# Kernel tuning notes

Hardware: AMD Instinct MI355X
Metric: run time of the kernel (lower is better)

Reference implementation:

```python
import jax, jax.numpy as jnp
import numpy as np

N = 50000
E = 800000
IN_DIM = 6
HID = 32
HEADS = 2
NEG_SLOPE = 0.2


def setup_inputs() -> dict:
    key = jax.random.key(0)
    ks = jax.random.split(key, 12)
    x = jax.random.normal(ks[0], (N, IN_DIM), dtype=jnp.float32)
    edge_index = jax.random.randint(ks[1], (2, E), 0, N, dtype=jnp.int64)
    s = 0.1
    W1 = jax.random.normal(ks[2], (IN_DIM, HEADS * HID), jnp.float32) * s
    a_src1 = jax.random.normal(ks[3], (HEADS, HID), jnp.float32) * s
    a_dst1 = jax.random.normal(ks[4], (HEADS, HID), jnp.float32) * s
    b1 = jnp.zeros((HEADS * HID,), jnp.float32)
    W2 = jax.random.normal(ks[5], (HEADS * HID, HID), jnp.float32) * s
    a_src2 = jax.random.normal(ks[6], (1, HID), jnp.float32) * s
    a_dst2 = jax.random.normal(ks[7], (1, HID), jnp.float32) * s
    b2 = jnp.zeros((HID,), jnp.float32)
    Wout = jax.random.normal(ks[8], (HID, 1), jnp.float32) * s
    bout = jnp.zeros((1,), jnp.float32)
    return {"x": x, "edge_index": edge_index, "W1": W1, "a_src1": a_src1,
            "a_dst1": a_dst1, "b1": b1, "W2": W2, "a_src2": a_src2,
            "a_dst2": a_dst2, "b2": b2, "Wout": Wout, "bout": bout}


def gat_conv(x, src, dst, n, W, a_src, a_dst, b, heads, out_ch, concat):
    # x: [N, F_in]; src/dst: [E'] (self-loops already appended)
    h = (x @ W).reshape(n, heads, out_ch)              # [N, H, C]
    alpha_s = jnp.sum(h * a_src, axis=-1)              # [N, H]
    alpha_d = jnp.sum(h * a_dst, axis=-1)              # [N, H]
    e = jax.nn.leaky_relu(alpha_s[src] + alpha_d[dst], NEG_SLOPE)  # [E', H]
    # segment softmax over incoming edges of each destination node
    m = jax.ops.segment_max(e, dst, num_segments=n)    # [N, H]
    ex = jnp.exp(e - m[dst])
    denom = jax.ops.segment_sum(ex, dst, num_segments=n)
    alpha = ex / denom[dst]                            # [E', H]
    out = jax.ops.segment_sum(alpha[:, :, None] * h[src], dst, num_segments=n)  # [N, H, C]
    out = out.reshape(n, heads * out_ch) if concat else out.mean(axis=1)
    return out + b


def reference(x, edge_index, W1, a_src1, a_dst1, b1, W2, a_src2, a_dst2, b2, Wout, bout):
    n = x.shape[0]
    loops = jnp.arange(n, dtype=edge_index.dtype)
    src = jnp.concatenate([edge_index[0], loops])
    dst = jnp.concatenate([edge_index[1], loops])
    h = jax.nn.relu(gat_conv(x, src, dst, n, W1, a_src1, a_dst1, b1, HEADS, HID, True))
    h = jax.nn.relu(gat_conv(h, src, dst, n, W2, a_src2, a_dst2, b2, 1, HID, False))
    return jax.nn.sigmoid(h @ Wout + bout).squeeze(-1)  # [N]
```

## Files before the change

kernel.cpp:

```cpp
#include <hip/hip_runtime.h>
#include <hip/hip_fp16.h>

#define N_NODES 50000
#define N_EDGES 800000
#define ETOT    (N_EDGES + N_NODES)
#define NEG_SLOPE 0.2f
#define NBIN    ((N_NODES + 255) / 256)
#define CHUNK   4096
#define B_COARSE ((ETOT + CHUNK - 1) / CHUNK)
#define G_NODE1 ((N_NODES + 3) / 4)
#define NG1     (N_NODES / 16)

__device__ __forceinline__ float leaky(float v) {
    return v > 0.f ? v : NEG_SLOPE * v;
}

__device__ __forceinline__ void edge_src_dst(const int* ei, int e, int& src, int& dst) {
    if (e < N_EDGES) { src = ei[e]; dst = ei[N_EDGES + e]; }
    else             { src = dst = e - N_EDGES; }
}

__global__ void k_pre(const float* __restrict__ x, const float* __restrict__ W1,
                      const float* __restrict__ a_src1, const float* __restrict__ a_dst1,
                      float* __restrict__ xs1, float* __restrict__ ad1,
                      const int* __restrict__ ei, int* __restrict__ bh) {
    __shared__ int h[NBIN];
    if (blockIdx.x < G_NODE1) {
        int node = blockIdx.x * 4 + (threadIdx.x >> 6);
        if (node >= N_NODES) return;
        int j = threadIdx.x & 63;
        int head = j >> 5;
        float xk[6];
#pragma unroll
        for (int k = 0; k < 6; ++k)
            xk[k] = x[node * 6 + k];
        float hv = 0.f;
#pragma unroll
        for (int k = 0; k < 6; ++k)
            hv += xk[k] * W1[k * 64 + j];
        float s = hv * a_src1[j];
        float d = hv * a_dst1[j];
#pragma unroll
        for (int m = 1; m < 32; m <<= 1) {
            s += __shfl_xor(s, m);
            d += __shfl_xor(d, m);
        }
        if ((j & 31) == 0) {
            xs1[node * 8 + head] = s;
            ad1[node * 2 + head] = d;
        }
        if (j >= 2 && j < 8)
            xs1[node * 8 + j] = xk[j - 2];
    } else {
        int b = blockIdx.x - G_NODE1;
        for (int i = threadIdx.x; i < NBIN; i += 256) h[i] = 0;
        __syncthreads();
        int base = b * CHUNK;
        int lim = min(base + CHUNK, ETOT);
        for (int e = base + threadIdx.x; e < lim; e += 256) {
            int s, d; edge_src_dst(ei, e, s, d);
            atomicAdd(&h[d >> 8], 1);
        }
        __syncthreads();
        for (int i = threadIdx.x; i < NBIN; i += 256)
            bh[b * NBIN + i] = h[i];
    }
}

__global__ void k_cscan_a(int* __restrict__ bh, int* __restrict__ bintot) {
    __shared__ int s[256];
    int bin = blockIdx.x;
    int t = threadIdx.x;
    int v = (t < B_COARSE) ? bh[t * NBIN + bin] : 0;
    int x = v;
    s[t] = x;
    __syncthreads();
#pragma unroll
    for (int o = 1; o < 256; o <<= 1) {
        int tt = (t >= o) ? s[t - o] : 0;
        __syncthreads();
        x += tt;
        s[t] = x;
        __syncthreads();
    }
    if (t < B_COARSE) bh[t * NBIN + bin] = x - v;
    if (t == 255) bintot[bin] = x;
}

__global__ void k_cscan_b(const int* __restrict__ bintot, int* __restrict__ binoff) {
    __shared__ int s[256];
    int t = threadIdx.x;
    int v = (t < NBIN) ? bintot[t] : 0;
    int x = v;
    s[t] = x;
    __syncthreads();
#pragma unroll
    for (int o = 1; o < 256; o <<= 1) {
        int tt = (t >= o) ? s[t - o] : 0;
        __syncthreads();
        x += tt;
        s[t] = x;
        __syncthreads();
    }
    if (t < NBIN) binoff[t] = x - v;
    if (t == 255) binoff[NBIN] = x;
}

__global__ void k_cscatter(const int* __restrict__ ei, const int* __restrict__ bh,
                           const int* __restrict__ binoff, unsigned* __restrict__ ebin) {
    __shared__ int cur[NBIN];
    for (int i = threadIdx.x; i < NBIN; i += 256)
        cur[i] = bh[blockIdx.x * NBIN + i] + binoff[i];
    __syncthreads();
    int base = blockIdx.x * CHUNK;
    int lim = min(base + CHUNK, ETOT);
    for (int e = base + threadIdx.x; e < lim; e += 256) {
        int s, d; edge_src_dst(ei, e, s, d);
        int pos = atomicAdd(&cur[d >> 8], 1);
        ebin[pos] = ((unsigned)s << 8) | (unsigned)(d & 255);
    }
}

__global__ void k_fine(const unsigned* __restrict__ ebin, const int* __restrict__ binoff,
                       int* __restrict__ rowstart, int* __restrict__ csr_src) {
    __shared__ int h[256];
    __shared__ int cur[256];
    int bin = blockIdx.x;
    int beg = binoff[bin], end = binoff[bin + 1];
    int t = threadIdx.x;
    h[t] = 0;
    __syncthreads();
    for (int i = beg + t; i < end; i += 256)
        atomicAdd(&h[ebin[i] & 255u], 1);
    __syncthreads();
    int v = h[t];
    int x = v;
    cur[t] = x;
    __syncthreads();
#pragma unroll
    for (int o = 1; o < 256; o <<= 1) {
        int tt = (t >= o) ? cur[t - o] : 0;
        __syncthreads();
        x += tt;
        cur[t] = x;
        __syncthreads();
    }
    int start = beg + x - v;
    int node = bin * 256 + t;
    if (node < N_NODES) rowstart[node] = start;
    if (bin == NBIN - 1 && t == 0) rowstart[N_NODES] = ETOT;
    cur[t] = start;
    __syncthreads();
    for (int i = beg + t; i < end; i += 256) {
        unsigned p = ebin[i];
        int pos = atomicAdd(&cur[p & 255u], 1);
        csr_src[pos] = (int)(p >> 8);
    }
}

__global__ void k_gat12(const int* __restrict__ csr_src, const int* __restrict__ rowstart,
                        const float* __restrict__ xs1, const float* __restrict__ ad1,
                        const float* __restrict__ W1, const float* __restrict__ b1,
                        const float* __restrict__ W2, const float* __restrict__ as_w2,
                        const float* __restrict__ ad_w2, __half* __restrict__ h2h,
                        float* __restrict__ as2, float* __restrict__ ad2) {
    __shared__ float W2s[64 * 32];
    __shared__ float o1s[16 * 66];
    int t = threadIdx.x;
    for (int i = t; i < 64 * 32; i += 256)
        W2s[i] = W2[i];

    int l = t & 15;
    int ln = t >> 4;
    int node = blockIdx.x * 16 + ln;

    float p[4][6];
    float bv[4];
#pragma unroll
    for (int m = 0; m < 4; ++m) {
        int c = l + 16 * m;
#pragma unroll
        for (int k = 0; k < 6; ++k)
            p[m][k] = W1[k * 64 + c];
        bv[m] = b1[c];
    }

    int beg = rowstart[node], end = rowstart[node + 1];
    float2 adv = ((const float2*)ad1)[node];

    float a0 = 0, a1 = 0, a2 = 0, a3 = 0, a4 = 0, a5 = 0;
    float c0 = 0, c1 = 0, c2 = 0, c3 = 0, c4 = 0, c5 = 0;
    float dp0 = 0, dp1 = 0;
    for (int i = beg + l; i < end; i += 16) {
        int s = csr_src[i];
        const float4* xp = (const float4*)(xs1 + (size_t)s * 8);
        float4 A = xp[0], B = xp[1];
        float w0 = __expf(leaky(A.x + adv.x));
        float w1 = __expf(leaky(A.y + adv.y));
        dp0 += w0;
        dp1 += w1;
        a0 += w0 * A.z; a1 += w0 * A.w; a2 += w0 * B.x;
        a3 += w0 * B.y; a4 += w0 * B.z; a5 += w0 * B.w;
        c0 += w1 * A.z; c1 += w1 * A.w; c2 += w1 * B.x;
        c3 += w1 * B.y; c4 += w1 * B.z; c5 += w1 * B.w;
    }
#pragma unroll
    for (int o = 8; o; o >>= 1) {
        a0 += __shfl_xor(a0, o); a1 += __shfl_xor(a1, o); a2 += __shfl_xor(a2, o);
        a3 += __shfl_xor(a3, o); a4 += __shfl_xor(a4, o); a5 += __shfl_xor(a5, o);
        c0 += __shfl_xor(c0, o); c1 += __shfl_xor(c1, o); c2 += __shfl_xor(c2, o);
        c3 += __shfl_xor(c3, o); c4 += __shfl_xor(c4, o); c5 += __shfl_xor(c5, o);
        dp0 += __shfl_xor(dp0, o); dp1 += __shfl_xor(dp1, o);
    }
    float inv0 = 1.f / dp0;
    float inv1 = 1.f / dp1;
#pragma unroll
    for (int m = 0; m < 4; ++m) {
        float dot;
        if (m < 2)
            dot = a0 * p[m][0] + a1 * p[m][1] + a2 * p[m][2]
                + a3 * p[m][3] + a4 * p[m][4] + a5 * p[m][5];
        else
            dot = c0 * p[m][0] + c1 * p[m][1] + c2 * p[m][2]
                + c3 * p[m][3] + c4 * p[m][4] + c5 * p[m][5];
        float v = dot * (m < 2 ? inv0 : inv1) + bv[m];
        o1s[ln * 66 + l + 16 * m] = v > 0.f ? v : 0.f;
    }
    __syncthreads();

    float h0 = 0.f, h1 = 0.f;
#pragma unroll
    for (int k = 0; k < 64; ++k) {
        float ov = o1s[ln * 66 + k];
        h0 += ov * W2s[k * 32 + l];
        h1 += ov * W2s[k * 32 + l + 16];
    }
    h2h[node * 32 + l] = __float2half(h0);
    h2h[node * 32 + l + 16] = __float2half(h1);
    float s2 = h0 * as_w2[l] + h1 * as_w2[l + 16];
    float d2 = h0 * ad_w2[l] + h1 * ad_w2[l + 16];
#pragma unroll
    for (int o = 8; o; o >>= 1) {
        s2 += __shfl_xor(s2, o);
        d2 += __shfl_xor(d2, o);
    }
    if (l == 0) {
        as2[node] = s2;
        ad2[node] = d2;
    }
}

__global__ void k_gat2(const int* __restrict__ csr_src, const int* __restrict__ rowstart,
                       const float* __restrict__ as2, const float* __restrict__ ad2,
                       const __half2* __restrict__ h2h, const float* __restrict__ b2,
                       const float* __restrict__ Wout, const float* __restrict__ bout,
                       float* __restrict__ out) {
    int node = blockIdx.x * 4 + (threadIdx.x >> 6);
    if (node >= N_NODES) return;
    int j = threadIdx.x & 63;
    int f = j & 15;
    int slot = j >> 4;
    int beg = rowstart[node], end = rowstart[node + 1];
    float adv = ad2[node];

    float accx = 0.f, accy = 0.f, dp = 0.f;
    for (int base = beg; base < end; base += 64) {
        int idx = base + j;
        float w = 0.f;
        int s = 0;
        if (idx < end) {
            s = csr_src[idx];
            w = __expf(leaky(as2[s] + adv));
            dp += w;
        }
        int cnt = min(64, end - base);
        for (int k = 0; k < cnt; k += 4) {
            int   sk = __shfl(s, k + slot);
            float wk = __shfl(w, k + slot);
            float2 hv = __half22float2(h2h[sk * 16 + f]);
            accx += wk * hv.x;
            accy += wk * hv.y;
        }
    }
#pragma unroll
    for (int o = 32; o; o >>= 1)
        dp += __shfl_xor(dp, o);
    accx += __shfl_xor(accx, 16); accy += __shfl_xor(accy, 16);
    accx += __shfl_xor(accx, 32); accy += __shfl_xor(accy, 32);

    float inv = 1.f / dp;
    float vx = accx * inv + b2[2 * f];
    float vy = accy * inv + b2[2 * f + 1];
    vx = vx > 0.f ? vx : 0.f;
    vy = vy > 0.f ? vy : 0.f;
    float t = vx * Wout[2 * f] + vy * Wout[2 * f + 1];
#pragma unroll
    for (int o = 8; o; o >>= 1)
        t += __shfl_xor(t, o);
    if (j == 0)
        out[node] = 1.f / (1.f + __expf(-(t + bout[0])));
}

extern "C" void kernel_launch(void* const* d_in, const int* in_sizes, int n_in,
                              void* d_out, int out_size, void* d_ws, size_t ws_size,
                              hipStream_t stream) {
    const float* x    = (const float*)d_in[0];
    const int*   ei   = (const int*)  d_in[1];
    const float* W1   = (const float*)d_in[2];
    const float* asw1 = (const float*)d_in[3];
    const float* adw1 = (const float*)d_in[4];
    const float* b1   = (const float*)d_in[5];
    const float* W2   = (const float*)d_in[6];
    const float* asw2 = (const float*)d_in[7];
    const float* adw2 = (const float*)d_in[8];
    const float* b2   = (const float*)d_in[9];
    const float* Wout = (const float*)d_in[10];
    const float* bout = (const float*)d_in[11];
    float* out = (float*)d_out;

    char* p = (char*)d_ws;
    auto carve = [&](size_t bytes) {
        void* r = (void*)p;
        p += (bytes + 255) & ~size_t(255);
        return r;
    };
    float*    xs1      = (float*)   carve((size_t)N_NODES * 8 * 4);
    __half*   h2h      = (__half*)  carve((size_t)N_NODES * 32 * 2);
    float*    ad1      = (float*)   carve((size_t)N_NODES * 2 * 4);
    float*    as2      = (float*)   carve((size_t)N_NODES * 4);
    float*    ad2      = (float*)   carve((size_t)N_NODES * 4);
    int*      bh       = (int*)     carve((size_t)B_COARSE * NBIN * 4);
    int*      bintot   = (int*)     carve((size_t)NBIN * 4);
    int*      binoff   = (int*)     carve((size_t)(NBIN + 1) * 4);
    unsigned* ebin     = (unsigned*)carve((size_t)ETOT * 4);
    int*      rowstart = (int*)     carve((size_t)(N_NODES + 1) * 4);
    int*      csr_src  = (int*)     carve((size_t)ETOT * 4);

    const int TB = 256;

    k_pre     <<<G_NODE1 + B_COARSE, TB, 0, stream>>>(x, W1, asw1, adw1, xs1, ad1, ei, bh);
    k_cscan_a <<<NBIN, TB, 0, stream>>>(bh, bintot);
    k_cscan_b <<<1, TB, 0, stream>>>(bintot, binoff);
    k_cscatter<<<B_COARSE, TB, 0, stream>>>(ei, bh, binoff, ebin);
    k_fine    <<<NBIN, TB, 0, stream>>>(ebin, binoff, rowstart, csr_src);

    k_gat12<<<NG1, TB, 0, stream>>>(csr_src, rowstart, xs1, ad1, W1, b1,
                                    W2, asw2, adw2, h2h, as2, ad2);

    k_gat2 <<<(N_NODES + 3) / 4, TB, 0, stream>>>(csr_src, rowstart, as2, ad2,
                                                  (const __half2*)h2h, b2, Wout, bout, out);
}
```

Baseline: 96.01 us.

## Aggregate GAT layers per coarse bin with shared-memory atomics, dropping fine CSR sort

Removes the fine-grained per-node CSR construction kernel. Both GAT layers now process the coarse 256-node bins directly, one block per bin, accumulating softmax numerators and denominators in LDS with atomicAdd. This drops a kernel launch and the rowstart/csr_src memory traffic. In exchange it runs only about 196 blocks on a large GPU and relies on heavy shared-memory float atomics, which can cost parallelism and contention.

```diff
diff --git a/kernel.cpp b/kernel.cpp
--- a/kernel.cpp
+++ b/kernel.cpp
@@ -9,7 +9,6 @@
 #define CHUNK   4096
 #define B_COARSE ((ETOT + CHUNK - 1) / CHUNK)
 #define G_NODE1 ((N_NODES + 3) / 4)
-#define NG1     (N_NODES / 16)
 
 __device__ __forceinline__ float leaky(float v) {
     return v > 0.f ? v : NEG_SLOPE * v;
@@ -121,61 +120,23 @@
     }
 }
 
-__global__ void k_fine(const unsigned* __restrict__ ebin, const int* __restrict__ binoff,
-                       int* __restrict__ rowstart, int* __restrict__ csr_src) {
-    __shared__ int h[256];
-    __shared__ int cur[256];
+__global__ __launch_bounds__(512) void k_gat1bin(
+    const unsigned* __restrict__ ebin, const int* __restrict__ binoff,
+    const float* __restrict__ xs1, const float* __restrict__ ad1,
+    const float* __restrict__ W1, const float* __restrict__ b1,
+    const float* __restrict__ W2, const float* __restrict__ as_w2,
+    const float* __restrict__ ad_w2, __half* __restrict__ h2h,
+    float* __restrict__ as2, float* __restrict__ ad2) {
+    __shared__ float accD[256 * 15];
+    __shared__ float o1s[32 * 66];
+    __shared__ float W2s[64 * 32];
+    int t = threadIdx.x;
     int bin = blockIdx.x;
-    int beg = binoff[bin], end = binoff[bin + 1];
-    int t = threadIdx.x;
-    h[t] = 0;
-    __syncthreads();
-    for (int i = beg + t; i < end; i += 256)
-        atomicAdd(&h[ebin[i] & 255u], 1);
-    __syncthreads();
-    int v = h[t];
-    int x = v;
-    cur[t] = x;
-    __syncthreads();
-#pragma unroll
-    for (int o = 1; o < 256; o <<= 1) {
-        int tt = (t >= o) ? cur[t - o] : 0;
-        __syncthreads();
-        x += tt;
-        cur[t] = x;
-        __syncthreads();
-    }
-    int start = beg + x - v;
-    int node = bin * 256 + t;
-    if (node < N_NODES) rowstart[node] = start;
-    if (bin == NBIN - 1 && t == 0) rowstart[N_NODES] = ETOT;
-    cur[t] = start;
-    __syncthreads();
-    for (int i = beg + t; i < end; i += 256) {
-        unsigned p = ebin[i];
-        int pos = atomicAdd(&cur[p & 255u], 1);
-        csr_src[pos] = (int)(p >> 8);
-    }
-}
-
-__global__ void k_gat12(const int* __restrict__ csr_src, const int* __restrict__ rowstart,
-                        const float* __restrict__ xs1, const float* __restrict__ ad1,
-                        const float* __restrict__ W1, const float* __restrict__ b1,
-                        const float* __restrict__ W2, const float* __restrict__ as_w2,
-                        const float* __restrict__ ad_w2, __half* __restrict__ h2h,
-                        float* __restrict__ as2, float* __restrict__ ad2) {
-    __shared__ float W2s[64 * 32];
-    __shared__ float o1s[16 * 66];
-    int t = threadIdx.x;
-    for (int i = t; i < 64 * 32; i += 256)
-        W2s[i] = W2[i];
+    for (int i = t; i < 256 * 15; i += 512) accD[i] = 0.f;
+    for (int i = t; i < 64 * 32; i += 512) W2s[i] = W2[i];
 
     int l = t & 15;
-    int ln = t >> 4;
-    int node = blockIdx.x * 16 + ln;
-
-    float p[4][6];
-    float bv[4];
+    float p[4][6], bv[4];
 #pragma unroll
     for (int m = 0; m < 4; ++m) {
         int c = l + 16 * m;
@@ -184,121 +145,114 @@
             p[m][k] = W1[k * 64 + c];
         bv[m] = b1[c];
     }
-
-    int beg = rowstart[node], end = rowstart[node + 1];
-    float2 adv = ((const float2*)ad1)[node];
-
-    float a0 = 0, a1 = 0, a2 = 0, a3 = 0, a4 = 0, a5 = 0;
-    float c0 = 0, c1 = 0, c2 = 0, c3 = 0, c4 = 0, c5 = 0;
-    float dp0 = 0, dp1 = 0;
-    for (int i = beg + l; i < end; i += 16) {
-        int s = csr_src[i];
+    __syncthreads();
+
+    int beg = binoff[bin], end = binoff[bin + 1];
+    const float2* ad1f2 = (const float2*)ad1;
+    for (int i = beg + t; i < end; i += 512) {
+        unsigned e = ebin[i];
+        int s = (int)(e >> 8);
+        int d = (int)(e & 255u);
+        float2 adv = ad1f2[bin * 256 + d];
         const float4* xp = (const float4*)(xs1 + (size_t)s * 8);
         float4 A = xp[0], B = xp[1];
         float w0 = __expf(leaky(A.x + adv.x));
         float w1 = __expf(leaky(A.y + adv.y));
-        dp0 += w0;
-        dp1 += w1;
-        a0 += w0 * A.z; a1 += w0 * A.w; a2 += w0 * B.x;
-        a3 += w0 * B.y; a4 += w0 * B.z; a5 += w0 * B.w;
-        c0 += w1 * A.z; c1 += w1 * A.w; c2 += w1 * B.x;
-        c3 += w1 * B.y; c4 += w1 * B.z; c5 += w1 * B.w;
-    }
-#pragma unroll
-    for (int o = 8; o; o >>= 1) {
-        a0 += __shfl_xor(a0, o); a1 += __shfl_xor(a1, o); a2 += __shfl_xor(a2, o);
-        a3 += __shfl_xor(a3, o); a4 += __shfl_xor(a4, o); a5 += __shfl_xor(a5, o);
-        c0 += __shfl_xor(c0, o); c1 += __shfl_xor(c1, o); c2 += __shfl_xor(c2, o);
-        c3 += __shfl_xor(c3, o); c4 += __shfl_xor(c4, o); c5 += __shfl_xor(c5, o);
-        dp0 += __shfl_xor(dp0, o); dp1 += __shfl_xor(dp1, o);
-    }
-    float inv0 = 1.f / dp0;
-    float inv1 = 1.f / dp1;
-#pragma unroll
-    for (int m = 0; m < 4; ++m) {
-        float dot;
-        if (m < 2)
-            dot = a0 * p[m][0] + a1 * p[m][1] + a2 * p[m][2]
-                + a3 * p[m][3] + a4 * p[m][4] + a5 * p[m][5];
-        else
-            dot = c0 * p[m][0] + c1 * p[m][1] + c2 * p[m][2]
-                + c3 * p[m][3] + c4 * p[m][4] + c5 * p[m][5];
-        float v = dot * (m < 2 ? inv0 : inv1) + bv[m];
-        o1s[ln * 66 + l + 16 * m] = v > 0.f ? v : 0.f;
-    }
-    __syncthreads();
-
-    float h0 = 0.f, h1 = 0.f;
-#pragma unroll
-    for (int k = 0; k < 64; ++k) {
-        float ov = o1s[ln * 66 + k];
-        h0 += ov * W2s[k * 32 + l];
-        h1 += ov * W2s[k * 32 + l + 16];
-    }
-    h2h[node * 32 + l] = __float2half(h0);
-    h2h[node * 32 + l + 16] = __float2half(h1);
-    float s2 = h0 * as_w2[l] + h1 * as_w2[l + 16];
-    float d2 = h0 * ad_w2[l] + h1 * ad_w2[l + 16];
-#pragma unroll
-    for (int o = 8; o; o >>= 1) {
-        s2 += __shfl_xor(s2, o);
-        d2 += __shfl_xor(d2, o);
-    }
-    if (l == 0) {
-        as2[node] = s2;
-        ad2[node] = d2;
-    }
-}
-
-__global__ void k_gat2(const int* __restrict__ csr_src, const int* __restrict__ rowstart,
-                       const float* __restrict__ as2, const float* __restrict__ ad2,
-                       const __half2* __restrict__ h2h, const float* __restrict__ b2,
-                       const float* __restrict__ Wout, const float* __restrict__ bout,
-                       float* __restrict__ out) {
-    int node = blockIdx.x * 4 + (threadIdx.x >> 6);
-    if (node >= N_NODES) return;
-    int j = threadIdx.x & 63;
-    int f = j & 15;
-    int slot = j >> 4;
-    int beg = rowstart[node], end = rowstart[node + 1];
-    float adv = ad2[node];
-
-    float accx = 0.f, accy = 0.f, dp = 0.f;
-    for (int base = beg; base < end; base += 64) {
-        int idx = base + j;
-        float w = 0.f;
-        int s = 0;
-        if (idx < end) {
-            s = csr_src[idx];
-            w = __expf(leaky(as2[s] + adv));
-            dp += w;
-        }
-        int cnt = min(64, end - base);
-        for (int k = 0; k < cnt; k += 4) {
-            int   sk = __shfl(s, k + slot);
-            float wk = __shfl(w, k + slot);
-            float2 hv = __half22float2(h2h[sk * 16 + f]);
-            accx += wk * hv.x;
-            accy += wk * hv.y;
-        }
-    }
-#pragma unroll
-    for (int o = 32; o; o >>= 1)
-        dp += __shfl_xor(dp, o);
-    accx += __shfl_xor(accx, 16); accy += __shfl_xor(accy, 16);
-    accx += __shfl_xor(accx, 32); accy += __shfl_xor(accy, 32);
-
-    float inv = 1.f / dp;
-    float vx = accx * inv + b2[2 * f];
-    float vy = accy * inv + b2[2 * f + 1];
-    vx = vx > 0.f ? vx : 0.f;
-    vy = vy > 0.f ? vy : 0.f;
-    float t = vx * Wout[2 * f] + vy * Wout[2 * f + 1];
-#pragma unroll
-    for (int o = 8; o; o >>= 1)
-        t += __shfl_xor(t, o);
-    if (j == 0)
-        out[node] = 1.f / (1.f + __expf(-(t + bout[0])));
+        float* r = accD + d * 15;
+        atomicAdd(r + 0, w0);          atomicAdd(r + 1, w1);
+        atomicAdd(r + 2, w0 * A.z);    atomicAdd(r + 3, w0 * A.w);
+        atomicAdd(r + 4, w0 * B.x);    atomicAdd(r + 5, w0 * B.y);
+        atomicAdd(r + 6, w0 * B.z);    atomicAdd(r + 7, w0 * B.w);
+        atomicAdd(r + 8, w1 * A.z);    atomicAdd(r + 9, w1 * A.w);
+        atomicAdd(r + 10, w1 * B.x);   atomicAdd(r + 11, w1 * B.y);
+        atomicAdd(r + 12, w1 * B.z);   atomicAdd(r + 13, w1 * B.w);
+    }
+    __syncthreads();
+
+    int ln = t >> 4;
+    for (int sub = 0; sub < 8; ++sub) {
+        int nl = sub * 32 + ln;
+        int node = bin * 256 + nl;
+        const float* r = accD + nl * 15;
+        float inv0 = 1.f / r[0];
+        float inv1 = 1.f / r[1];
+#pragma unroll
+        for (int m = 0; m < 4; ++m) {
+            const float* xr = (m < 2) ? (r + 2) : (r + 8);
+            float dot = xr[0] * p[m][0] + xr[1] * p[m][1] + xr[2] * p[m][2]
+                      + xr[3] * p[m][3] + xr[4] * p[m][4] + xr[5] * p[m][5];
+            float v = dot * (m < 2 ? inv0 : inv1) + bv[m];
+            o1s[ln * 66 + l + 16 * m] = v > 0.f ? v : 0.f;
+        }
+        __syncthreads();
+        float h0 = 0.f, h1 = 0.f;
+#pragma unroll
+        for (int k = 0; k < 64; ++k) {
+            float ov = o1s[ln * 66 + k];
+            h0 += ov * W2s[k * 32 + l];
+            h1 += ov * W2s[k * 32 + l + 16];
+        }
+        float s2 = h0 * as_w2[l] + h1 * as_w2[l + 16];
+        float d2 = h0 * ad_w2[l] + h1 * ad_w2[l + 16];
+#pragma unroll
+        for (int o = 8; o; o >>= 1) {
+            s2 += __shfl_xor(s2, o);
+            d2 += __shfl_xor(d2, o);
+        }
+        if (node < N_NODES) {
+            h2h[node * 32 + l] = __float2half(h0);
+            h2h[node * 32 + l + 16] = __float2half(h1);
+            if (l == 0) { as2[node] = s2; ad2[node] = d2; }
+        }
+        __syncthreads();
+    }
+}
+
+__global__ __launch_bounds__(512) void k_gat2bin(
+    const unsigned* __restrict__ ebin, const int* __restrict__ binoff,
+    const float* __restrict__ as2, const float* __restrict__ ad2,
+    const __half2* __restrict__ h2h2, const float* __restrict__ b2,
+    const float* __restrict__ Wout, const float* __restrict__ bout,
+    float* __restrict__ out) {
+    __shared__ float acc2[256 * 33];
+    __shared__ float b2s[32], wos[32];
+    int t = threadIdx.x;
+    int bin = blockIdx.x;
+    for (int i = t; i < 256 * 33; i += 512) acc2[i] = 0.f;
+    if (t < 32) { b2s[t] = b2[t]; wos[t] = Wout[t]; }
+    __syncthreads();
+
+    int beg = binoff[bin], end = binoff[bin + 1];
+    int g = t >> 4;
+    int f = t & 15;
+    for (int i = beg + g; i < end; i += 32) {
+        unsigned e = ebin[i];
+        int s = (int)(e >> 8);
+        int d = (int)(e & 255u);
+        float w = __expf(leaky(as2[s] + ad2[bin * 256 + d]));
+        float2 hv = __half22float2(h2h2[s * 16 + f]);
+        float* r = acc2 + d * 33;
+        atomicAdd(r + 2 * f, w * hv.x);
+        atomicAdd(r + 2 * f + 1, w * hv.y);
+        if (f == 0) atomicAdd(r + 32, w);
+    }
+    __syncthreads();
+
+    if (t < 256) {
+        int node = bin * 256 + t;
+        if (node < N_NODES) {
+            const float* r = acc2 + t * 33;
+            float inv = 1.f / r[32];
+            float acc = 0.f;
+#pragma unroll
+            for (int k = 0; k < 32; ++k) {
+                float v = r[k] * inv + b2s[k];
+                v = v > 0.f ? v : 0.f;
+                acc += v * wos[k];
+            }
+            out[node] = 1.f / (1.f + __expf(-(acc + bout[0])));
+        }
+    }
 }
 
 extern "C" void kernel_launch(void* const* d_in, const int* in_sizes, int n_in,
@@ -333,8 +287,6 @@
     int*      bintot   = (int*)     carve((size_t)NBIN * 4);
     int*      binoff   = (int*)     carve((size_t)(NBIN + 1) * 4);
     unsigned* ebin     = (unsigned*)carve((size_t)ETOT * 4);
-    int*      rowstart = (int*)     carve((size_t)(N_NODES + 1) * 4);
-    int*      csr_src  = (int*)     carve((size_t)ETOT * 4);
 
     const int TB = 256;
 
@@ -342,11 +294,10 @@
     k_cscan_a <<<NBIN, TB, 0, stream>>>(bh, bintot);
     k_cscan_b <<<1, TB, 0, stream>>>(bintot, binoff);
     k_cscatter<<<B_COARSE, TB, 0, stream>>>(ei, bh, binoff, ebin);
-    k_fine    <<<NBIN, TB, 0, stream>>>(ebin, binoff, rowstart, csr_src);
-
-    k_gat12<<<NG1, TB, 0, stream>>>(csr_src, rowstart, xs1, ad1, W1, b1,
-                                    W2, asw2, adw2, h2h, as2, ad2);
-
-    k_gat2 <<<(N_NODES + 3) / 4, TB, 0, stream>>>(csr_src, rowstart, as2, ad2,
-                                                  (const __half2*)h2h, b2, Wout, bout, out);
-}
+
+    k_gat1bin<<<NBIN, 512, 0, stream>>>(ebin, binoff, xs1, ad1, W1, b1,
+                                        W2, asw2, adw2, h2h, as2, ad2);
+
+    k_gat2bin<<<NBIN, 512, 0, stream>>>(ebin, binoff, as2, ad2,
+                                        (const __half2*)h2h, b2, Wout, bout, out);
+}
```

After: 331.0 us. 3.45x slower.

## Replace per-block histogram scans with global atomic bin totals and cursors

Applied to the files above, without the earlier changes.

The coarse counting-sort now accumulates per-bin counts into a global array with atomics instead of storing a per-block histogram, which removes the two scan kernels. Each scatter block recounts its own chunk's histogram, scans the global totals locally, and claims its slot range with an atomic on a global cursor. The fine kernel recomputes bin offsets from the totals itself. This cuts two kernel launches and the scan traffic, but the scatter kernel reads the edges twice, and the edge order inside each bin is no longer deterministic.

```diff
diff --git a/kernel.cpp b/kernel.cpp
--- a/kernel.cpp
+++ b/kernel.cpp
@@ -23,7 +23,7 @@
 __global__ void k_pre(const float* __restrict__ x, const float* __restrict__ W1,
                       const float* __restrict__ a_src1, const float* __restrict__ a_dst1,
                       float* __restrict__ xs1, float* __restrict__ ad1,
-                      const int* __restrict__ ei, int* __restrict__ bh) {
+                      const int* __restrict__ ei, int* __restrict__ bintot) {
     __shared__ int h[NBIN];
     if (blockIdx.x < G_NODE1) {
         int node = blockIdx.x * 4 + (threadIdx.x >> 6);
@@ -63,32 +63,53 @@
         }
         __syncthreads();
         for (int i = threadIdx.x; i < NBIN; i += 256)
-            bh[b * NBIN + i] = h[i];
-    }
-}
-
-__global__ void k_cscan_a(int* __restrict__ bh, int* __restrict__ bintot) {
+            if (h[i]) atomicAdd(&bintot[i], h[i]);
+    }
+}
+
+__global__ void k_cscatter(const int* __restrict__ ei, const int* __restrict__ bintot,
+                           int* __restrict__ gcur, unsigned* __restrict__ ebin) {
+    __shared__ int hcnt[NBIN];
+    __shared__ int s[256];
+    __shared__ int cur[NBIN];
+    int t = threadIdx.x;
+    for (int i = t; i < NBIN; i += 256) hcnt[i] = 0;
+    __syncthreads();
+    int base = blockIdx.x * CHUNK;
+    int lim = min(base + CHUNK, ETOT);
+    for (int e = base + t; e < lim; e += 256) {
+        int sv, d; edge_src_dst(ei, e, sv, d);
+        atomicAdd(&hcnt[d >> 8], 1);
+    }
+    __syncthreads();
+    int v = (t < NBIN) ? bintot[t] : 0;
+    int x = v;
+    s[t] = x;
+    __syncthreads();
+#pragma unroll
+    for (int o = 1; o < 256; o <<= 1) {
+        int tt = (t >= o) ? s[t - o] : 0;
+        __syncthreads();
+        x += tt;
+        s[t] = x;
+        __syncthreads();
+    }
+    if (t < NBIN)
+        cur[t] = (x - v) + atomicAdd(&gcur[t], hcnt[t]);
+    __syncthreads();
+    for (int e = base + t; e < lim; e += 256) {
+        int sv, d; edge_src_dst(ei, e, sv, d);
+        int pos = atomicAdd(&cur[d >> 8], 1);
+        ebin[pos] = ((unsigned)sv << 8) | (unsigned)(d & 255);
+    }
+}
+
+__global__ void k_fine(const unsigned* __restrict__ ebin, const int* __restrict__ bintot,
+                       int* __restrict__ rowstart, int* __restrict__ csr_src) {
+    __shared__ int h[256];
+    __shared__ int cur[256];
     __shared__ int s[256];
     int bin = blockIdx.x;
-    int t = threadIdx.x;
-    int v = (t < B_COARSE) ? bh[t * NBIN + bin] : 0;
-    int x = v;
-    s[t] = x;
-    __syncthreads();
-#pragma unroll
-    for (int o = 1; o < 256; o <<= 1) {
-        int tt = (t >= o) ? s[t - o] : 0;
-        __syncthreads();
-        x += tt;
-        s[t] = x;
-        __syncthreads();
-    }
-    if (t < B_COARSE) bh[t * NBIN + bin] = x - v;
-    if (t == 255) bintot[bin] = x;
-}
-
-__global__ void k_cscan_b(const int* __restrict__ bintot, int* __restrict__ binoff) {
-    __shared__ int s[256];
     int t = threadIdx.x;
     int v = (t < NBIN) ? bintot[t] : 0;
     int x = v;
@@ -102,50 +123,27 @@
         s[t] = x;
         __syncthreads();
     }
-    if (t < NBIN) binoff[t] = x - v;
-    if (t == 255) binoff[NBIN] = x;
-}
-
-__global__ void k_cscatter(const int* __restrict__ ei, const int* __restrict__ bh,
-                           const int* __restrict__ binoff, unsigned* __restrict__ ebin) {
-    __shared__ int cur[NBIN];
-    for (int i = threadIdx.x; i < NBIN; i += 256)
-        cur[i] = bh[blockIdx.x * NBIN + i] + binoff[i];
-    __syncthreads();
-    int base = blockIdx.x * CHUNK;
-    int lim = min(base + CHUNK, ETOT);
-    for (int e = base + threadIdx.x; e < lim; e += 256) {
-        int s, d; edge_src_dst(ei, e, s, d);
-        int pos = atomicAdd(&cur[d >> 8], 1);
-        ebin[pos] = ((unsigned)s << 8) | (unsigned)(d & 255);
-    }
-}
-
-__global__ void k_fine(const unsigned* __restrict__ ebin, const int* __restrict__ binoff,
-                       int* __restrict__ rowstart, int* __restrict__ csr_src) {
-    __shared__ int h[256];
-    __shared__ int cur[256];
-    int bin = blockIdx.x;
-    int beg = binoff[bin], end = binoff[bin + 1];
-    int t = threadIdx.x;
+    s[t] = x;
     h[t] = 0;
     __syncthreads();
+    int beg = (bin == 0) ? 0 : s[bin - 1];
+    int end = s[bin];
     for (int i = beg + t; i < end; i += 256)
         atomicAdd(&h[ebin[i] & 255u], 1);
     __syncthreads();
-    int v = h[t];
-    int x = v;
-    cur[t] = x;
+    int hv = h[t];
+    int xx = hv;
+    cur[t] = xx;
     __syncthreads();
 #pragma unroll
     for (int o = 1; o < 256; o <<= 1) {
         int tt = (t >= o) ? cur[t - o] : 0;
         __syncthreads();
-        x += tt;
-        cur[t] = x;
-        __syncthreads();
-    }
-    int start = beg + x - v;
+        xx += tt;
+        cur[t] = xx;
+        __syncthreads();
+    }
+    int start = beg + xx - hv;
     int node = bin * 256 + t;
     if (node < N_NODES) rowstart[node] = start;
     if (bin == NBIN - 1 && t == 0) rowstart[N_NODES] = ETOT;
@@ -329,20 +327,19 @@
     float*    ad1      = (float*)   carve((size_t)N_NODES * 2 * 4);
     float*    as2      = (float*)   carve((size_t)N_NODES * 4);
     float*    ad2      = (float*)   carve((size_t)N_NODES * 4);
-    int*      bh       = (int*)     carve((size_t)B_COARSE * NBIN * 4);
-    int*      bintot   = (int*)     carve((size_t)NBIN * 4);
-    int*      binoff   = (int*)     carve((size_t)(NBIN + 1) * 4);
+    int*      bintot   = (int*)     carve((size_t)NBIN * 2 * 4);
+    int*      gcur     = bintot + NBIN;
     unsigned* ebin     = (unsigned*)carve((size_t)ETOT * 4);
     int*      rowstart = (int*)     carve((size_t)(N_NODES + 1) * 4);
     int*      csr_src  = (int*)     carve((size_t)ETOT * 4);
 
     const int TB = 256;
 
-    k_pre     <<<G_NODE1 + B_COARSE, TB, 0, stream>>>(x, W1, asw1, adw1, xs1, ad1, ei, bh);
-    k_cscan_a <<<NBIN, TB, 0, stream>>>(bh, bintot);
-    k_cscan_b <<<1, TB, 0, stream>>>(bintot, binoff);
-    k_cscatter<<<B_COARSE, TB, 0, stream>>>(ei, bh, binoff, ebin);
-    k_fine    <<<NBIN, TB, 0, stream>>>(ebin, binoff, rowstart, csr_src);
+    hipMemsetAsync(bintot, 0, (size_t)NBIN * 2 * 4, stream);
+
+    k_pre     <<<G_NODE1 + B_COARSE, TB, 0, stream>>>(x, W1, asw1, adw1, xs1, ad1, ei, bintot);
+    k_cscatter<<<B_COARSE, TB, 0, stream>>>(ei, bintot, gcur, ebin);
+    k_fine    <<<NBIN, TB, 0, stream>>>(ebin, bintot, rowstart, csr_src);
 
     k_gat12<<<NG1, TB, 0, stream>>>(csr_src, rowstart, xs1, ad1, W1, b1,
                                     W2, asw2, adw2, h2h, as2, ad2);
```

After: 108.3 us. 12.8% more time.
